# Kernel optimization log

Measured on AMD Instinct MI355X. Metric: run time of the kernel, lower is better.

The kernel has to match this reference:

```python
import jax, jax.numpy as jnp
import numpy as np

NUM_HEADS = 16


def setup_inputs() -> dict:
    key = jax.random.key(0)
    k1, k2, k3 = jax.random.split(key, 3)
    B, S, D = 2, 2048, 1024
    x = jax.random.normal(k1, (B, S, D), dtype=jnp.float32)
    # qkv_bias=False -> no bias on qkv projection; output Dense has default bias
    w_qkv = jax.random.normal(k2, (D, 3 * D), dtype=jnp.float32) * (1.0 / np.sqrt(D))
    w_out = jax.random.normal(k3, (D, D), dtype=jnp.float32) * (1.0 / np.sqrt(D))
    b_out = jnp.zeros((D,), dtype=jnp.float32)
    return {"x": x, "w_qkv": w_qkv, "w_out": w_out, "b_out": b_out}


def reference(x, w_qkv, w_out, b_out):
    B, S, D = x.shape
    H = NUM_HEADS
    Dh = D // H
    scale = 1.0 / np.sqrt(Dh).astype(np.float32)

    qkv = jnp.einsum('bsd,de->bse', x, w_qkv)           # [B,S,3D]
    q, k, v = jnp.split(qkv, 3, axis=-1)
    split = lambda t: t.reshape(B, S, H, Dh).transpose(0, 2, 1, 3)  # [B,H,S,Dh]
    q, k, v = split(q), split(k), split(v)

    attn = jnp.einsum('bhid,bhjd->bhij', q, k) * scale  # [B,H,S,S]
    # mask=None -> all-ones mask combined with causal mask => causal float mask
    causal = jnp.tril(jnp.ones((S, S), dtype=jnp.float32))[None, None]
    attn = causal * attn + (1.0 - causal) * (-1e9)
    attn = jax.nn.softmax(attn, axis=-1)

    out = jnp.einsum('bhij,bhjd->bhid', attn, v)        # [B,H,S,Dh]
    out = out.transpose(0, 2, 1, 3).reshape(B, S, D)    # merge heads
    return jnp.einsum('bsd,de->bse', out, w_out) + b_out
```

## Files before the change

kernel.cpp:

```cpp
#include <hip/hip_runtime.h>

typedef unsigned short u16;
typedef __bf16 bf16x8 __attribute__((ext_vector_type(8)));
typedef unsigned short u16x8 __attribute__((ext_vector_type(8)));
typedef float f32x4 __attribute__((ext_vector_type(4)));

union Frag { u16x8 u; bf16x8 b; };

__device__ __forceinline__ u16 f2bf(float f) {
  unsigned u = __builtin_bit_cast(unsigned, f);
  u += 0x7fff + ((u >> 16) & 1);
  return (u16)(u >> 16);
}

__device__ __forceinline__ f32x4 mfma16(bf16x8 a, bf16x8 b, f32x4 c) {
  return __builtin_amdgcn_mfma_f32_16x16x32_bf16(a, b, c, 0, 0, 0);
}

__device__ __forceinline__ float exp2_raw(float x) {
  float r;
  asm("v_exp_f32 %0, %1" : "=v"(r) : "v"(x));
  return r;
}

typedef const __attribute__((address_space(1))) void* as1cv;
typedef __attribute__((address_space(3))) void* as3v;

__device__ __forceinline__ void glds16(const u16* g, u16* l) {
  __builtin_amdgcn_global_load_lds((as1cv)g, (as3v)l, 16, 0, 0);
}

__global__ __launch_bounds__(256) void prep(const float* __restrict__ x,
                                            u16* __restrict__ xb,
                                            const float* __restrict__ wqkv,
                                            u16* __restrict__ wqkvT,
                                            const float* __restrict__ wout,
                                            u16* __restrict__ woutT) {
  __shared__ float tile[32][33];
  int bid = blockIdx.x;
  int tid = threadIdx.x;
  if (bid >= 4096) {
    int i = (bid - 4096) * 256 + tid;
    const int stride = 1024 * 256;
#pragma unroll
    for (int k = 0; k < 4; ++k) {
      float4 v = ((const float4*)x)[i];
      ushort4 o;
      o.x = f2bf(v.x); o.y = f2bf(v.y); o.z = f2bf(v.z); o.w = f2bf(v.w);
      ((ushort4*)xb)[i] = o;
      i += stride;
    }
    return;
  }
  const float* src; u16* dst; int N;
  if (bid < 3072) { src = wqkv; dst = wqkvT; N = 3072; }
  else            { bid -= 3072; src = wout; dst = woutT; N = 1024; }
  const int K = 1024;
  int tn = N >> 5;
  int bk = bid / tn, bn = bid % tn;
  int k0 = bk << 5, n0 = bn << 5;
  int tx = tid & 31, ty = tid >> 5;
#pragma unroll
  for (int i = 0; i < 4; i++)
    tile[ty + 8 * i][tx] = src[(size_t)(k0 + ty + 8 * i) * N + n0 + tx];
  __syncthreads();
#pragma unroll
  for (int i = 0; i < 4; i++)
    dst[(size_t)(n0 + ty + 8 * i) * K + k0 + tx] = f2bf(tile[tx][ty + 8 * i]);
}

__global__ __launch_bounds__(256) void gemm_qkv(const u16* __restrict__ A,
                                                const u16* __restrict__ BT,
                                                u16* __restrict__ C,
                                                u16* __restrict__ vt,
                                                int N, int K, int nbc) {
  __shared__ u16 Al[2][128 * 32];
  __shared__ u16 Bl[2][128 * 32];
  int nwg = gridDim.x;
  int bid = blockIdx.x;
  int swz = (bid & 7) * (nwg >> 3) + (bid >> 3);
  int br = swz / nbc, bc = swz % nbc;
  int tid = threadIdx.x;
  int w = tid >> 6, l = tid & 63;
  int lg = l >> 4, lq = l & 15;
  int wr = w >> 1, wc = w & 1;

  f32x4 acc[4][4];
#pragma unroll
  for (int m = 0; m < 4; m++)
#pragma unroll
    for (int n = 0; n < 4; n++)
      acc[m][n] = (f32x4){0.f, 0.f, 0.f, 0.f};

  const u16* Ab = A + (size_t)(br * 128 + 32 * w + (l >> 2)) * K + (l & 3) * 8;
  const u16* Bb = BT + (size_t)(bc * 128 + 32 * w + (l >> 2)) * K + (l & 3) * 8;

  auto stage = [&](int it, int buf) {
    int kt = it * 32;
    u16* ald = &Al[buf][32 * w * 32];
    u16* bld = &Bl[buf][32 * w * 32];
    glds16(Ab + kt, ald);
    glds16(Ab + (size_t)16 * K + kt, ald + 16 * 32);
    glds16(Bb + kt, bld);
    glds16(Bb + (size_t)16 * K + kt, bld + 16 * 32);
  };

  int nk = K >> 5;
  stage(0, 0);
  __syncthreads();

  for (int it = 0; it < nk; ++it) {
    int buf = it & 1;
    if (it + 1 < nk) stage(it + 1, buf ^ 1);

    Frag af[4], bf[4];
#pragma unroll
    for (int m = 0; m < 4; m++)
      af[m].u = *(const u16x8*)(&Al[buf][(64 * wr + 16 * m + lq) * 32 + lg * 8]);
#pragma unroll
    for (int n = 0; n < 4; n++)
      bf[n].u = *(const u16x8*)(&Bl[buf][(64 * wc + 16 * n + lq) * 32 + lg * 8]);
    __builtin_amdgcn_s_setprio(1);
#pragma unroll
    for (int m = 0; m < 4; m++)
#pragma unroll
      for (int n = 0; n < 4; n++)
        acc[m][n] = mfma16(af[m].b, bf[n].b, acc[m][n]);
    __builtin_amdgcn_s_setprio(0);
    __syncthreads();
  }

  int row0 = br * 128 + 64 * wr + lg * 4;
  int col0 = bc * 128 + 64 * wc + lq;
  if (bc < 16) {
#pragma unroll
    for (int n = 0; n < 4; n++)
#pragma unroll
      for (int m = 0; m < 4; m++)
#pragma unroll
        for (int r = 0; r < 4; r++)
          C[(size_t)(row0 + 16 * m + r) * N + col0 + 16 * n] = f2bf(acc[m][n][r]);
  } else {
#pragma unroll
    for (int n = 0; n < 4; n++) {
      int vcol = col0 + 16 * n - 2048;
      int h = vcol >> 6, dh = vcol & 63;
#pragma unroll
      for (int m = 0; m < 4; m++) {
        int s_abs = row0 + 16 * m;
        int bb = s_abs >> 11;
        int s = s_abs & 2047;
        int e = (s >> 5) * 32 + ((s >> 4) & 1) * 4 + ((s >> 2) & 3) * 8;
        ushort4 v;
        v.x = f2bf(acc[m][n][0]); v.y = f2bf(acc[m][n][1]);
        v.z = f2bf(acc[m][n][2]); v.w = f2bf(acc[m][n][3]);
        *(ushort4*)&vt[((size_t)(bb * 16 + h) * 64 + dh) * 2048 + e] = v;
      }
    }
  }
}

__global__ __launch_bounds__(256) void gemm_bt(const u16* __restrict__ A,
                                               const u16* __restrict__ BT,
                                               float* __restrict__ Cout,
                                               const float* __restrict__ bias,
                                               int N, int K, int nbc) {
  __shared__ u16 Al[2][128 * 32];
  __shared__ u16 Bl[2][128 * 32];
  int nwg = gridDim.x;
  int bid = blockIdx.x;
  int swz = (bid & 7) * (nwg >> 3) + (bid >> 3);
  int br = swz / nbc, bc = swz % nbc;
  int tid = threadIdx.x;
  int w = tid >> 6, l = tid & 63;
  int lg = l >> 4, lq = l & 15;
  int wr = w >> 1, wc = w & 1;

  f32x4 acc[4][4];
#pragma unroll
  for (int m = 0; m < 4; m++)
#pragma unroll
    for (int n = 0; n < 4; n++)
      acc[m][n] = (f32x4){0.f, 0.f, 0.f, 0.f};

  const u16* Ab = A + (size_t)(br * 128 + 32 * w + (l >> 2)) * K + (l & 3) * 8;
  const u16* Bb = BT + (size_t)(bc * 128 + 32 * w + (l >> 2)) * K + (l & 3) * 8;

  auto stage = [&](int it, int buf) {
    int kt = it * 32;
    u16* ald = &Al[buf][32 * w * 32];
    u16* bld = &Bl[buf][32 * w * 32];
    glds16(Ab + kt, ald);
    glds16(Ab + (size_t)16 * K + kt, ald + 16 * 32);
    glds16(Bb + kt, bld);
    glds16(Bb + (size_t)16 * K + kt, bld + 16 * 32);
  };

  int nk = K >> 5;
  stage(0, 0);
  __syncthreads();

  for (int it = 0; it < nk; ++it) {
    int buf = it & 1;
    if (it + 1 < nk) stage(it + 1, buf ^ 1);

    Frag af[4], bf[4];
#pragma unroll
    for (int m = 0; m < 4; m++)
      af[m].u = *(const u16x8*)(&Al[buf][(64 * wr + 16 * m + lq) * 32 + lg * 8]);
#pragma unroll
    for (int n = 0; n < 4; n++)
      bf[n].u = *(const u16x8*)(&Bl[buf][(64 * wc + 16 * n + lq) * 32 + lg * 8]);
    __builtin_amdgcn_s_setprio(1);
#pragma unroll
    for (int m = 0; m < 4; m++)
#pragma unroll
      for (int n = 0; n < 4; n++)
        acc[m][n] = mfma16(af[m].b, bf[n].b, acc[m][n]);
    __builtin_amdgcn_s_setprio(0);
    __syncthreads();
  }

  int row0 = br * 128 + 64 * wr + lg * 4;
  int col0 = bc * 128 + 64 * wc + lq;
#pragma unroll
  for (int n = 0; n < 4; n++) {
    float bv = bias[col0 + 16 * n];
#pragma unroll
    for (int m = 0; m < 4; m++)
#pragma unroll
      for (int r = 0; r < 4; r++)
        Cout[(size_t)(row0 + 16 * m + r) * N + col0 + 16 * n] = acc[m][n][r] + bv;
  }
}

__global__ __launch_bounds__(256) void flash_attn(const u16* __restrict__ qkv,
                                                  const u16* __restrict__ vt,
                                                  u16* __restrict__ aout) {
  __shared__ __align__(16) u16 pool[2][8192];
  const float SL2E = 0.18033688011112043f;
  int bid = blockIdx.x;
  int bh = bid & 31;
  int g = bid >> 5;
  int qb = (g < 8) ? (31 - g) : (g < 16) ? (g - 8) : (g < 24) ? (39 - g) : (g - 16);
  int b = bh >> 4, h = bh & 15;
  int tid = threadIdx.x;
  int w = tid >> 6, l = tid & 63;
  int lg = l >> 4, lq = l & 15;
  int q0w = qb * 64 + w * 16;
  int qidx = q0w + lq;
  int ntiles = qb + 1;

  const size_t rs = 3072;
  int srw = l >> 3;
  int scol = 8 * ((l & 7) ^ srw);
  const u16* kg = qkv + (size_t)(b * 2048) * rs + 1024 + h * 64;
  const u16* vg = vt + (size_t)bh * 64 * 2048;
  int r0 = (w * 2 + 0) * 8 + srw;
  int r1 = (w * 2 + 1) * 8 + srw;
  int swz = (lq & 7) << 3;

  Frag qf0, qf1;
  const u16* qbase = qkv + (size_t)(b * 2048 + q0w + lq) * rs + h * 64 + lg * 8;
  qf0.u = *(const u16x8*)(qbase);
  qf1.u = *(const u16x8*)(qbase + 32);

  float lam = 0.f;
  f32x4 o[4];
#pragma unroll
  for (int d = 0; d < 4; ++d) o[d] = (f32x4){0.f, 0.f, 0.f, 0.f};

  auto stage = [&](int tile, int buf) {
    int kt2 = tile * 64;
    u16* nb = &pool[buf][0];
    glds16(kg + (size_t)(kt2 + r0) * rs + scol, nb + (w * 2 + 0) * 512);
    glds16(kg + (size_t)(kt2 + r1) * rs + scol, nb + (w * 2 + 1) * 512);
    glds16(vg + (size_t)r0 * 2048 + kt2 + scol, nb + 4096 + (w * 2 + 0) * 512);
    glds16(vg + (size_t)r1 * 2048 + kt2 + scol, nb + 4096 + (w * 2 + 1) * 512);
  };

  stage(0, 0);
  __syncthreads();

  for (int t = 0; t < ntiles; ++t) {
    if (t + 1 < ntiles) stage(t + 1, (t + 1) & 1);
    const u16* Kl = &pool[t & 1][0];
    const u16* Vl = &pool[t & 1][4096];
    int kt = t * 64;

    f32x4 s[4];
    __builtin_amdgcn_s_setprio(1);
#pragma unroll
    for (int sub = 0; sub < 4; ++sub) {
      int row = sub * 16 + lq;
      Frag k0, k1;
      k0.u = *(const u16x8*)(Kl + row * 64 + ((lg * 8) ^ swz));
      k1.u = *(const u16x8*)(Kl + row * 64 + ((32 + lg * 8) ^ swz));
      f32x4 z = {0.f, 0.f, 0.f, 0.f};
      s[sub] = mfma16(k0.b, qf0.b, z);
      s[sub] = mfma16(k1.b, qf1.b, s[sub]);
    }
    __builtin_amdgcn_s_setprio(0);

    if (t == qb) {
#pragma unroll
      for (int sub = 0; sub < 4; ++sub)
#pragma unroll
        for (int r = 0; r < 4; ++r) {
          int key = kt + sub * 16 + lg * 4 + r;
          if (key > qidx) s[sub][r] = -1e30f;
        }
    }

    Frag pf[2];
#pragma unroll
    for (int hf = 0; hf < 2; ++hf)
#pragma unroll
      for (int r = 0; r < 4; ++r) {
        float p0 = exp2_raw(s[2 * hf][r] * SL2E);
        float p1 = exp2_raw(s[2 * hf + 1][r] * SL2E);
        lam += p0 + p1;
        pf[hf].b[r] = (__bf16)p0;
        pf[hf].b[4 + r] = (__bf16)p1;
      }

    __builtin_amdgcn_s_setprio(1);
#pragma unroll
    for (int d = 0; d < 4; ++d) {
      int row = d * 16 + lq;
      Frag vf0, vf1;
      vf0.u = *(const u16x8*)(Vl + row * 64 + ((lg * 8) ^ swz));
      vf1.u = *(const u16x8*)(Vl + row * 64 + ((32 + lg * 8) ^ swz));
      o[d] = mfma16(vf0.b, pf[0].b, o[d]);
      o[d] = mfma16(vf1.b, pf[1].b, o[d]);
    }
    __builtin_amdgcn_s_setprio(0);
    __syncthreads();
  }

  lam += __shfl_xor(lam, 16);
  lam += __shfl_xor(lam, 32);
  float inv = 1.0f / lam;

  u16* Ost = &pool[0][0] + w * (16 * 72);
#pragma unroll
  for (int d = 0; d < 4; ++d)
#pragma unroll
    for (int r = 0; r < 4; ++r)
      Ost[lq * 72 + d * 16 + lg * 4 + r] = f2bf(o[d][r] * inv);
  int q = l >> 2, c16 = (l & 3) * 16;
  u16x8 t0, t1;
#pragma unroll
  for (int j = 0; j < 8; j++) { t0[j] = Ost[q * 72 + c16 + j]; t1[j] = Ost[q * 72 + c16 + 8 + j]; }
  u16* orow = aout + (size_t)(b * 2048 + qb * 64 + w * 16 + q) * 1024 + h * 64 + c16;
  *(u16x8*)orow = t0;
  *(u16x8*)(orow + 8) = t1;
}

extern "C" void kernel_launch(void* const* d_in, const int* in_sizes, int n_in,
                              void* d_out, int out_size, void* d_ws, size_t ws_size,
                              hipStream_t stream) {
  const float* x    = (const float*)d_in[0];
  const float* wqkv = (const float*)d_in[1];
  const float* wout = (const float*)d_in[2];
  const float* bout = (const float*)d_in[3];
  float* out = (float*)d_out;

  char* ws = (char*)d_ws;
  u16* xb    = (u16*)(ws);
  u16* wqkvT = (u16*)(ws + 8388608);
  u16* woutT = (u16*)(ws + 14680064);
  u16* qkvb  = (u16*)(ws + 16777216);
  u16* vtb   = (u16*)(ws + 41943040);
  u16* aoutb = (u16*)(ws + 50331648);

  prep<<<5120, 256, 0, stream>>>(x, xb, wqkv, wqkvT, wout, woutT);

  gemm_qkv<<<(4096 / 128) * (3072 / 128), 256, 0, stream>>>(xb, wqkvT, qkvb, vtb,
                                                            3072, 1024, 3072 / 128);
  flash_attn<<<1024, 256, 0, stream>>>(qkvb, vtb, aoutb);

  gemm_bt<<<(4096 / 128) * (1024 / 128), 256, 0, stream>>>(aoutb, woutT, out, bout,
                                                           1024, 1024, 1024 / 128);
}
```

Before: 102.6 us.

## Triple-buffer GEMM LDS staging with partial vmcnt waits instead of full syncs

Both bf16 GEMM kernels move from double to triple buffering of the A/B LDS tiles, so loads are issued two k-steps ahead. The full __syncthreads is replaced by an s_waitcnt vmcnt(4) plus a raw s_barrier, which keeps the next stage's loads in flight across the barrier. The goal is to hide global-to-LDS latency behind MFMA work. In exchange, LDS use per block grows by half, which may lower occupancy, and correctness depends on the hand-counted vmcnt values.

```diff
diff --git a/kernel.cpp b/kernel.cpp
--- a/kernel.cpp
+++ b/kernel.cpp
@@ -29,6 +29,8 @@
 __device__ __forceinline__ void glds16(const u16* g, u16* l) {
   __builtin_amdgcn_global_load_lds((as1cv)g, (as3v)l, 16, 0, 0);
 }
+
+#define FENCE asm volatile("" ::: "memory")
 
 __global__ __launch_bounds__(256) void prep(const float* __restrict__ x,
                                             u16* __restrict__ xb,
@@ -74,8 +76,8 @@
                                                 u16* __restrict__ C,
                                                 u16* __restrict__ vt,
                                                 int N, int K, int nbc) {
-  __shared__ u16 Al[2][128 * 32];
-  __shared__ u16 Bl[2][128 * 32];
+  __shared__ u16 Al[3][128 * 32];
+  __shared__ u16 Bl[3][128 * 32];
   int nwg = gridDim.x;
   int bid = blockIdx.x;
   int swz = (bid & 7) * (nwg >> 3) + (bid >> 3);
@@ -107,19 +109,22 @@
 
   int nk = K >> 5;
   stage(0, 0);
-  __syncthreads();
-
+  stage(1, 1);
+  asm volatile("s_waitcnt vmcnt(4)" ::: "memory");
+  FENCE; __builtin_amdgcn_s_barrier(); FENCE;
+
+  int cur = 0;
   for (int it = 0; it < nk; ++it) {
-    int buf = it & 1;
-    if (it + 1 < nk) stage(it + 1, buf ^ 1);
+    int b2 = cur + 2; if (b2 >= 3) b2 -= 3;
+    if (it + 2 < nk) stage(it + 2, b2);
 
     Frag af[4], bf[4];
 #pragma unroll
     for (int m = 0; m < 4; m++)
-      af[m].u = *(const u16x8*)(&Al[buf][(64 * wr + 16 * m + lq) * 32 + lg * 8]);
+      af[m].u = *(const u16x8*)(&Al[cur][(64 * wr + 16 * m + lq) * 32 + lg * 8]);
 #pragma unroll
     for (int n = 0; n < 4; n++)
-      bf[n].u = *(const u16x8*)(&Bl[buf][(64 * wc + 16 * n + lq) * 32 + lg * 8]);
+      bf[n].u = *(const u16x8*)(&Bl[cur][(64 * wc + 16 * n + lq) * 32 + lg * 8]);
     __builtin_amdgcn_s_setprio(1);
 #pragma unroll
     for (int m = 0; m < 4; m++)
@@ -127,7 +132,11 @@
       for (int n = 0; n < 4; n++)
         acc[m][n] = mfma16(af[m].b, bf[n].b, acc[m][n]);
     __builtin_amdgcn_s_setprio(0);
-    __syncthreads();
+
+    if (it + 2 < nk)      asm volatile("s_waitcnt vmcnt(4)" ::: "memory");
+    else if (it + 1 < nk) asm volatile("s_waitcnt vmcnt(0)" ::: "memory");
+    if (it + 1 < nk) { FENCE; __builtin_amdgcn_s_barrier(); FENCE; }
+    cur += 1; if (cur >= 3) cur -= 3;
   }
 
   int row0 = br * 128 + 64 * wr + lg * 4;
@@ -165,8 +174,8 @@
                                                float* __restrict__ Cout,
                                                const float* __restrict__ bias,
                                                int N, int K, int nbc) {
-  __shared__ u16 Al[2][128 * 32];
-  __shared__ u16 Bl[2][128 * 32];
+  __shared__ u16 Al[3][128 * 32];
+  __shared__ u16 Bl[3][128 * 32];
   int nwg = gridDim.x;
   int bid = blockIdx.x;
   int swz = (bid & 7) * (nwg >> 3) + (bid >> 3);
@@ -198,19 +207,22 @@
 
   int nk = K >> 5;
   stage(0, 0);
-  __syncthreads();
-
+  stage(1, 1);
+  asm volatile("s_waitcnt vmcnt(4)" ::: "memory");
+  FENCE; __builtin_amdgcn_s_barrier(); FENCE;
+
+  int cur = 0;
   for (int it = 0; it < nk; ++it) {
-    int buf = it & 1;
-    if (it + 1 < nk) stage(it + 1, buf ^ 1);
+    int b2 = cur + 2; if (b2 >= 3) b2 -= 3;
+    if (it + 2 < nk) stage(it + 2, b2);
 
     Frag af[4], bf[4];
 #pragma unroll
     for (int m = 0; m < 4; m++)
-      af[m].u = *(const u16x8*)(&Al[buf][(64 * wr + 16 * m + lq) * 32 + lg * 8]);
+      af[m].u = *(const u16x8*)(&Al[cur][(64 * wr + 16 * m + lq) * 32 + lg * 8]);
 #pragma unroll
     for (int n = 0; n < 4; n++)
-      bf[n].u = *(const u16x8*)(&Bl[buf][(64 * wc + 16 * n + lq) * 32 + lg * 8]);
+      bf[n].u = *(const u16x8*)(&Bl[cur][(64 * wc + 16 * n + lq) * 32 + lg * 8]);
     __builtin_amdgcn_s_setprio(1);
 #pragma unroll
     for (int m = 0; m < 4; m++)
@@ -218,7 +230,11 @@
       for (int n = 0; n < 4; n++)
         acc[m][n] = mfma16(af[m].b, bf[n].b, acc[m][n]);
     __builtin_amdgcn_s_setprio(0);
-    __syncthreads();
+
+    if (it + 2 < nk)      asm volatile("s_waitcnt vmcnt(4)" ::: "memory");
+    else if (it + 1 < nk) asm volatile("s_waitcnt vmcnt(0)" ::: "memory");
+    if (it + 1 < nk) { FENCE; __builtin_amdgcn_s_barrier(); FENCE; }
+    cur += 1; if (cur >= 3) cur -= 3;
   }
 
   int row0 = br * 128 + 64 * wr + lg * 4;
```

New measurement: 104.4 us. About the same (+1.7%).

## Stage V-transpose epilogue through LDS and tile V^T into contiguous 64x64 blocks

Applied to the files above, without the earlier changes.

The QKV GEMM epilogue for the V part now writes each wave's 64x64 accumulator tile into swizzled LDS, then reads it back transposed and emits 16-byte vector stores. Before, it issued scattered 8-byte stores. The V^T buffer layout becomes blocked, so each 64-key by 64-dh tile is contiguous, and the attention kernel's V staging loads change their addressing to match. The goal is coalesced, wider global writes and contiguous reads of V tiles, at the cost of extra LDS traffic and a reuse of the GEMM's shared buffers after the main loop.

```diff
diff --git a/kernel.cpp b/kernel.cpp
--- a/kernel.cpp
+++ b/kernel.cpp
@@ -141,21 +141,36 @@
         for (int r = 0; r < 4; r++)
           C[(size_t)(row0 + 16 * m + r) * N + col0 + 16 * n] = f2bf(acc[m][n][r]);
   } else {
-#pragma unroll
-    for (int n = 0; n < 4; n++) {
-      int vcol = col0 + 16 * n - 2048;
-      int h = vcol >> 6, dh = vcol & 63;
-#pragma unroll
-      for (int m = 0; m < 4; m++) {
-        int s_abs = row0 + 16 * m;
-        int bb = s_abs >> 11;
-        int s = s_abs & 2047;
-        int e = (s >> 5) * 32 + ((s >> 4) & 1) * 4 + ((s >> 2) & 3) * 8;
-        ushort4 v;
-        v.x = f2bf(acc[m][n][0]); v.y = f2bf(acc[m][n][1]);
-        v.z = f2bf(acc[m][n][2]); v.w = f2bf(acc[m][n][3]);
-        *(ushort4*)&vt[((size_t)(bb * 16 + h) * 64 + dh) * 2048 + e] = v;
+    u16* stbuf = (w == 0) ? &Al[0][0] : (w == 1) ? &Al[1][0]
+               : (w == 2) ? &Bl[0][0] : &Bl[1][0];
+#pragma unroll
+    for (int m = 0; m < 4; m++)
+#pragma unroll
+      for (int r = 0; r < 4; r++) {
+        int srow = 16 * m + 4 * lg + r;
+        int X = ((srow >> 2) & 7) << 3;
+#pragma unroll
+        for (int n = 0; n < 4; n++)
+          stbuf[srow * 64 + ((16 * n + lq) ^ X)] = f2bf(acc[m][n][r]);
       }
+    int a = l >> 3, bgrp = l & 7;
+    int s_base = br * 128 + 64 * wr;
+    int bb = s_base >> 11;
+    int sblk = (s_base & 2047) >> 6;
+    int hh = ((bc - 16) << 1) | wc;
+    size_t vbase = ((size_t)(bb * 16 + hh) * 32 + sblk) * 4096;
+#pragma unroll
+    for (int j = 0; j < 8; ++j) {
+      int dh = 8 * j + a;
+      u16x8 v;
+#pragma unroll
+      for (int i = 0; i < 8; ++i) {
+        int srow = ((bgrp >> 2) << 5) | (((i >> 2) & 1) << 4) |
+                   ((bgrp & 3) << 2) | (i & 3);
+        int X = ((srow >> 2) & 7) << 3;
+        v[i] = stbuf[srow * 64 + (dh ^ X)];
+      }
+      *(u16x8*)&vt[vbase + dh * 64 + bgrp * 8] = v;
     }
   }
 }
@@ -255,7 +270,7 @@
   int srw = l >> 3;
   int scol = 8 * ((l & 7) ^ srw);
   const u16* kg = qkv + (size_t)(b * 2048) * rs + 1024 + h * 64;
-  const u16* vg = vt + (size_t)bh * 64 * 2048;
+  const u16* vg = vt + (size_t)bh * 32 * 4096;
   int r0 = (w * 2 + 0) * 8 + srw;
   int r1 = (w * 2 + 1) * 8 + srw;
   int swz = (lq & 7) << 3;
@@ -275,8 +290,8 @@
     u16* nb = &pool[buf][0];
     glds16(kg + (size_t)(kt2 + r0) * rs + scol, nb + (w * 2 + 0) * 512);
     glds16(kg + (size_t)(kt2 + r1) * rs + scol, nb + (w * 2 + 1) * 512);
-    glds16(vg + (size_t)r0 * 2048 + kt2 + scol, nb + 4096 + (w * 2 + 0) * 512);
-    glds16(vg + (size_t)r1 * 2048 + kt2 + scol, nb + 4096 + (w * 2 + 1) * 512);
+    glds16(vg + (size_t)kt2 * 64 + r0 * 64 + scol, nb + 4096 + (w * 2 + 0) * 512);
+    glds16(vg + (size_t)kt2 * 64 + r1 * 64 + scol, nb + 4096 + (w * 2 + 1) * 512);
   };
 
   stage(0, 0);
```

New measurement: 103.0 us. Within noise of the previous version (+0.3%).
